# Performance work log

Hardware: AMD Instinct MI355X
Metric: run time of the kernel (lower is better)

Reference implementation:

```python
import jax, jax.numpy as jnp
import numpy as np

D_MODEL = 256
N_HEADS = 8
N_LEVELS = 3
N_POINTS = 4
D_HEAD = D_MODEL // N_HEADS
SHAPES = [(128, 128), (64, 64), (32, 32)]  # (H, W) per level
BS = 8
NQ = 900


def setup_inputs() -> dict:
    key = jax.random.key(0)
    ks = jax.random.split(key, 13)
    sum_hw = sum(h * w for h, w in SHAPES)
    s = 0.02
    starts = np.cumsum([0] + [h * w for h, w in SHAPES[:-1]]).astype(np.int32)
    return {
        "query": jax.random.normal(ks[0], (BS, NQ, D_MODEL), jnp.float32),
        "reference_points": jax.random.uniform(ks[1], (BS, NQ, N_LEVELS, 2), jnp.float32),
        "input_flatten": jax.random.normal(ks[2], (BS, sum_hw, D_MODEL), jnp.float32),
        "spatial_shapes": jnp.array(SHAPES, jnp.int32),
        "level_start_index": jnp.array(starts, jnp.int32),
        "W_off": jax.random.normal(ks[3], (D_MODEL, N_HEADS * N_LEVELS * N_POINTS * 2), jnp.float32) * s,
        "b_off": jax.random.normal(ks[4], (N_HEADS * N_LEVELS * N_POINTS * 2,), jnp.float32),
        "W_attn": jax.random.normal(ks[5], (D_MODEL, N_HEADS * N_LEVELS * N_POINTS), jnp.float32) * s,
        "b_attn": jax.random.normal(ks[6], (N_HEADS * N_LEVELS * N_POINTS,), jnp.float32) * s,
        "W_val": jax.random.normal(ks[7], (D_MODEL, D_MODEL), jnp.float32) * s,
        "b_val": jnp.zeros((D_MODEL,), jnp.float32),
        "W_out": jax.random.normal(ks[8], (D_MODEL, D_MODEL), jnp.float32) * s,
        "b_out": jnp.zeros((D_MODEL,), jnp.float32),
    }


def _msda(query, reference_points, input_flatten, shapes_np, starts_np,
          W_off, b_off, W_attn, b_attn, W_val, b_val, W_out, b_out):
    bs, nq, _ = query.shape
    # value projection -> [bs, sum_hw, H, Dh]
    value = (input_flatten @ W_val + b_val).reshape(bs, -1, N_HEADS, D_HEAD)
    # learned offsets and attention weights
    offsets = (query @ W_off + b_off).reshape(bs, nq, N_HEADS, N_LEVELS, N_POINTS, 2)
    attn = (query @ W_attn + b_attn).reshape(bs, nq, N_HEADS, N_LEVELS * N_POINTS)
    attn = jax.nn.softmax(attn, axis=-1).reshape(bs, nq, N_HEADS, N_LEVELS, N_POINTS)

    bidx = jnp.arange(bs)[:, None, None, None]
    hidx = jnp.arange(N_HEADS)[None, None, :, None]
    acc = jnp.zeros((bs, nq, N_HEADS, D_HEAD), value.dtype)
    for l in range(N_LEVELS):
        Hl, Wl = int(shapes_np[l, 0]), int(shapes_np[l, 1])
        st = int(starts_np[l])
        # [bs, H, Hl*Wl, Dh]
        v = jnp.transpose(value[:, st:st + Hl * Wl], (0, 2, 1, 3))
        norm = jnp.array([Wl, Hl], value.dtype)
        # sampling locations in [0,1] -> pixel coords (grid_sample align_corners=False)
        loc = reference_points[:, :, None, l, None, :] + offsets[:, :, :, l] / norm
        px = loc[..., 0] * Wl - 0.5  # [bs, nq, H, P]
        py = loc[..., 1] * Hl - 0.5
        x0 = jnp.floor(px); y0 = jnp.floor(py)
        lx = px - x0; ly = py - y0
        x0i = x0.astype(jnp.int32); y0i = y0.astype(jnp.int32)

        def gather(ix, iy):
            valid = (ix >= 0) & (ix < Wl) & (iy >= 0) & (iy < Hl)
            flat = jnp.clip(iy, 0, Hl - 1) * Wl + jnp.clip(ix, 0, Wl - 1)
            g = v[bidx, hidx, flat]  # [bs, nq, H, P, Dh]
            return g * valid[..., None].astype(v.dtype)

        samp = (gather(x0i, y0i) * ((1 - lx) * (1 - ly))[..., None]
                + gather(x0i + 1, y0i) * (lx * (1 - ly))[..., None]
                + gather(x0i, y0i + 1) * ((1 - lx) * ly)[..., None]
                + gather(x0i + 1, y0i + 1) * (lx * ly)[..., None])
        acc = acc + jnp.einsum('bqhp,bqhpd->bqhd', attn[:, :, :, l], samp)

    return acc.reshape(bs, nq, D_MODEL) @ W_out + b_out


def reference(query, reference_points, input_flatten, spatial_shapes, level_start_index,
              W_off, b_off, W_attn, b_attn, W_val, b_val, W_out, b_out):
    shapes_np = np.asarray(spatial_shapes)
    starts_np = np.asarray(level_start_index)
    return _msda(query, reference_points, input_flatten, shapes_np, starts_np,
                 W_off, b_off, W_attn, b_attn, W_val, b_val, W_out, b_out)
```

## Files before the change

kernel.cpp:

```cpp
#include <hip/hip_runtime.h>
#include <hip/hip_bf16.h>

typedef __bf16 bf16;
typedef bf16 bf16x8 __attribute__((ext_vector_type(8)));
typedef float f32x4 __attribute__((ext_vector_type(4)));

#define BSZ 8
#define NQ 900
#define NH 8
#define SUMHW 21504
#define NROW 7200

#define BIGF 3.3e38f

__device__ inline float ld_rt(const void* p, size_t i, int f32) {
  return f32 ? ((const float*)p)[i] : (float)((const bf16*)p)[i];
}

__device__ inline bf16x8 load_a8(const void* p, size_t i, int f32) {
  if (f32) {
    const float4* s = (const float4*)((const float*)p + i);
    float4 v0 = s[0], v1 = s[1];
    bf16x8 d;
    d[0] = (bf16)v0.x; d[1] = (bf16)v0.y; d[2] = (bf16)v0.z; d[3] = (bf16)v0.w;
    d[4] = (bf16)v1.x; d[5] = (bf16)v1.y; d[6] = (bf16)v1.z; d[7] = (bf16)v1.w;
    return d;
  }
  return *(const bf16x8*)((const bf16*)p + i);
}

__global__ void probe_flags(const bf16* q, int* flags) {
  const int lane = threadIdx.x;
  int c = 0;
  for (int i = lane; i < 512; i += 64) {
    float x = (float)q[i];
    if (!(fabsf(x) <= 1000.f)) c++;
  }
#pragma unroll
  for (int m = 1; m < 64; m <<= 1) c += __shfl_xor(c, m, 64);
  if (lane == 0) {
    flags[0] = (c > 32) ? 1 : 0;
    flags[1] = 0;
    flags[2] = 0;
  }
}

__global__ __launch_bounds__(256) void transpose256(const void* __restrict__ in,
                                                    bf16* __restrict__ out,
                                                    const int* __restrict__ flags) {
  const int f32 = flags[0];
  int idx = blockIdx.x * 256 + threadIdx.x;
  int k = idx >> 8, n = idx & 255;
  out[n * 256 + k] = (bf16)ld_rt(in, idx, f32);
}

__global__ __launch_bounds__(256) void transpose_oa(const void* __restrict__ Woff,
                                                    const void* __restrict__ Wattn,
                                                    bf16* __restrict__ Wt,
                                                    const int* __restrict__ flags) {
  const int f32 = flags[0];
  int idx = blockIdx.x * 256 + threadIdx.x;
  int n = idx >> 8, k = idx & 255;
  float v = (n < 192) ? ld_rt(Woff, (size_t)k * 192 + n, f32)
                      : ld_rt(Wattn, (size_t)k * 96 + (n - 192), f32);
  Wt[idx] = (bf16)v;
}

template <typename TC>
__global__ __launch_bounds__(256) void gemm_stream(
    const void* __restrict__ A, const bf16* __restrict__ Wt,
    const void* __restrict__ bias, TC* __restrict__ C, int rowbase, int M,
    const int* __restrict__ aflags, const int* __restrict__ bflags) {
  const int af32 = aflags[0], bf32 = bflags[0];
  const int t = threadIdx.x;
  const int w = t >> 6, lane = t & 63;
  const int ml = lane & 15, qd = lane >> 4;
  const int blockM = blockIdx.x * 64 + w * 16;
  f32x4 acc[16] = {};

  int r0 = blockM + ml;
  if (r0 > M - 1) r0 = M - 1;
  const size_t ar = ((size_t)rowbase + r0) * 256;

  for (int ks = 0; ks < 8; ++ks) {
    const int kof = ks * 32 + qd * 8;
    bf16x8 a = load_a8(A, ar + kof, af32);
#pragma unroll
    for (int tn = 0; tn < 16; ++tn) {
      bf16x8 bb = *(const bf16x8*)(Wt + (size_t)(tn * 16 + ml) * 256 + kof);
      acc[tn] = __builtin_amdgcn_mfma_f32_16x16x32_bf16(a, bb, acc[tn], 0, 0, 0);
    }
  }

#pragma unroll
  for (int tn = 0; tn < 16; ++tn) {
    int col = tn * 16 + ml;
    float bv = ld_rt(bias, col, bf32);
#pragma unroll
    for (int rr = 0; rr < 4; ++rr) {
      int row = blockM + qd * 4 + rr;
      float v = fminf(fmaxf(acc[tn][rr] + bv, -BIGF), BIGF);
      if (row < M) C[((size_t)rowbase + row) * 256 + col] = (TC)v;
    }
  }
}

__global__ __launch_bounds__(256) void gemm_oa_stream(
    const void* __restrict__ query, const bf16* __restrict__ Wt,
    const void* __restrict__ boff, const void* __restrict__ battn,
    float* __restrict__ offs, float* __restrict__ logits,
    const int* __restrict__ flags) {
  const int f32 = flags[0];
  const int t = threadIdx.x;
  const int w = t >> 6, lane = t & 63;
  const int ml = lane & 15, qd = lane >> 4;
  const int blockM = blockIdx.x * 64 + w * 16;
  f32x4 acc[18] = {};

  int r0 = blockM + ml;
  if (r0 > NROW - 1) r0 = NROW - 1;
  const size_t ar = (size_t)r0 * 256;

  for (int ks = 0; ks < 8; ++ks) {
    const int kof = ks * 32 + qd * 8;
    bf16x8 a = load_a8(query, ar + kof, f32);
#pragma unroll
    for (int tn = 0; tn < 18; ++tn) {
      bf16x8 bb = *(const bf16x8*)(Wt + (size_t)(tn * 16 + ml) * 256 + kof);
      acc[tn] = __builtin_amdgcn_mfma_f32_16x16x32_bf16(a, bb, acc[tn], 0, 0, 0);
    }
  }

#pragma unroll
  for (int tn = 0; tn < 18; ++tn) {
    int col = tn * 16 + ml;
#pragma unroll
    for (int rr = 0; rr < 4; ++rr) {
      int row = blockM + qd * 4 + rr;
      if (row < NROW) {
        float v = acc[tn][rr];
        if (col < 192)
          offs[(size_t)row * 192 + col] = v + ld_rt(boff, col, f32);
        else
          logits[(size_t)row * 96 + (col - 192)] = v + ld_rt(battn, col - 192, f32);
      }
    }
  }
}

__global__ __launch_bounds__(256) void msda_sample(
    const bf16* __restrict__ value, const void* __restrict__ refp,
    const float* __restrict__ offs, const float* __restrict__ logits,
    bf16* __restrict__ accb, int b_base, size_t batch_stride,
    const int* __restrict__ flags) {
  const int f32 = flags[0];
  const int qi = blockIdx.x, bl = blockIdx.y;
  const int b = b_base + bl;
  const int row = b * NQ + qi;
  const int t = threadIdx.x, h = t >> 5, d = t & 31;
  const bf16* valb = value + (size_t)bl * batch_stride;

  const float* lg = logits + (size_t)(row * NH + h) * 12;
  float lv[12];
#pragma unroll
  for (int i = 0; i < 12; ++i) lv[i] = fminf(fmaxf(lg[i], -BIGF), BIGF);
  float mx = -BIGF;
#pragma unroll
  for (int i = 0; i < 12; ++i) mx = fmaxf(mx, lv[i]);
  float e[12], se = 0.f;
#pragma unroll
  for (int i = 0; i < 12; ++i) {
    e[i] = __expf(lv[i] - mx);
    se += e[i];
  }
  const float inv = 1.f / se;

  const float* of = offs + (size_t)(row * NH + h) * 24;
  const int Hs[3] = {128, 64, 32}, Wd[3] = {128, 64, 32}, st[3] = {0, 16384, 20480};
  float acc = 0.f;
#pragma unroll
  for (int l = 0; l < 3; ++l) {
    const int Hl = Hs[l], Wl = Wd[l];
    float rx = ld_rt(refp, (size_t)(row * 3 + l) * 2 + 0, f32);
    float ry = ld_rt(refp, (size_t)(row * 3 + l) * 2 + 1, f32);
    const bf16* base = valb + (size_t)st[l] * 256 + h * 32 + d;
#pragma unroll
    for (int p = 0; p < 4; ++p) {
      float ox = of[(l * 4 + p) * 2 + 0], oy = of[(l * 4 + p) * 2 + 1];
      float px = (rx + ox / (float)Wl) * (float)Wl - 0.5f;
      float py = (ry + oy / (float)Hl) * (float)Hl - 0.5f;
      px = fminf(fmaxf(px, -1e6f), 1e6f);
      py = fminf(fmaxf(py, -1e6f), 1e6f);
      const float x0f = floorf(px), y0f = floorf(py);
      const float lx = px - x0f, ly = py - y0f;
      const int x0 = (int)x0f, y0 = (int)y0f;
      const float wgt = e[l * 4 + p] * inv;
      float s = 0.f;
#pragma unroll
      for (int cy = 0; cy < 2; ++cy) {
        const int iy = y0 + cy;
        const float wy = cy ? ly : 1.f - ly;
        const bool vy = (iy >= 0) && (iy < Hl);
        const int iyc = iy < 0 ? 0 : (iy > Hl - 1 ? Hl - 1 : iy);
#pragma unroll
        for (int cx = 0; cx < 2; ++cx) {
          const int ix = x0 + cx;
          const float wx = cx ? lx : 1.f - lx;
          const bool vx = (ix >= 0) && (ix < Wl);
          const int ixc = ix < 0 ? 0 : (ix > Wl - 1 ? Wl - 1 : ix);
          float g = (float)base[(size_t)(iyc * Wl + ixc) * 256];
          g = fminf(fmaxf(g, -BIGF), BIGF);
          s += (vx && vy) ? wx * wy * g : 0.f;
        }
      }
      acc += wgt * s;
    }
  }
  accb[(size_t)row * 256 + t] = (bf16)acc;
}

extern "C" void kernel_launch(void* const* d_in, const int* in_sizes, int n_in,
                              void* d_out, int out_size, void* d_ws, size_t ws_size,
                              hipStream_t stream) {
  const void* query = d_in[0];
  const void* refp = d_in[1];
  const void* inpf = d_in[2];
  const void* W_off = d_in[5];
  const void* b_off = d_in[6];
  const void* W_attn = d_in[7];
  const void* b_attn = d_in[8];
  const void* W_val = d_in[9];
  const void* b_val = d_in[10];
  const void* W_out = d_in[11];
  const void* b_out = d_in[12];

  float* out = (float*)d_out;
  char* ws = (char*)d_ws;
  int* flags = (int*)ws;
  const int* bf16flag = flags + 2;
  bf16* Wt_val = (bf16*)(ws + 256);
  bf16* Wt_out = (bf16*)(ws + 131328);
  bf16* Wt_oa = (bf16*)(ws + 262400);
  float* offs = (float*)(ws + 409856);
  float* logits = (float*)(ws + 5939456);
  bf16* accb = (bf16*)(ws + 8704256);
  bf16* value = (bf16*)(ws + 12390656);
  const unsigned long long WS_FULL = 12390656ULL + 88080384ULL;
  const unsigned long long WS_TIGHT = 12390656ULL + 11010048ULL;

  const int pipeline_ok = ws_size >= WS_TIGHT;
  const int full = ws_size >= WS_FULL;

  probe_flags<<<1, 64, 0, stream>>>((const bf16*)query, flags);
  if (pipeline_ok) {
    transpose256<<<256, 256, 0, stream>>>(W_val, Wt_val, flags);
    transpose256<<<256, 256, 0, stream>>>(W_out, Wt_out, flags);
    transpose_oa<<<288, 256, 0, stream>>>(W_off, W_attn, Wt_oa, flags);
    gemm_oa_stream<<<(NROW + 63) / 64, 256, 0, stream>>>(query, Wt_oa, b_off,
                                                         b_attn, offs, logits,
                                                         flags);
    if (full) {
      gemm_stream<bf16><<<(BSZ * SUMHW) / 64, 256, 0, stream>>>(
          inpf, Wt_val, b_val, value, 0, BSZ * SUMHW, flags, flags);
      msda_sample<<<dim3(NQ, BSZ), 256, 0, stream>>>(
          value, refp, offs, logits, accb, 0, (size_t)SUMHW * 256, flags);
    } else {
      for (int b = 0; b < BSZ; ++b) {
        gemm_stream<bf16><<<SUMHW / 64, 256, 0, stream>>>(
            inpf, Wt_val, b_val, value - (size_t)b * SUMHW * 256, b * SUMHW, SUMHW,
            flags, flags);
        msda_sample<<<dim3(NQ, 1), 256, 0, stream>>>(value, refp, offs, logits, accb,
                                                     b, 0, flags);
      }
    }
    gemm_stream<float><<<(NROW + 63) / 64, 256, 0, stream>>>(
        accb, Wt_out, b_out, out, 0, NROW, bf16flag, flags);
  }
}
```

Measured before the change: 566.7 us.

## Stage transposed weights in swizzled LDS and use persistent 512-thread GEMM blocks

```diff
diff --git a/kernel.cpp b/kernel.cpp
--- a/kernel.cpp
+++ b/kernel.cpp
@@ -67,82 +67,116 @@
 }
 
 template <typename TC>
-__global__ __launch_bounds__(256) void gemm_stream(
+__global__ __launch_bounds__(512, 2) void gemm_ldsb(
     const void* __restrict__ A, const bf16* __restrict__ Wt,
     const void* __restrict__ bias, TC* __restrict__ C, int rowbase, int M,
     const int* __restrict__ aflags, const int* __restrict__ bflags) {
+  extern __shared__ bf16 Bs[];
   const int af32 = aflags[0], bf32 = bflags[0];
   const int t = threadIdx.x;
   const int w = t >> 6, lane = t & 63;
   const int ml = lane & 15, qd = lane >> 4;
-  const int blockM = blockIdx.x * 64 + w * 16;
-  f32x4 acc[16] = {};
-
-  int r0 = blockM + ml;
-  if (r0 > M - 1) r0 = M - 1;
-  const size_t ar = ((size_t)rowbase + r0) * 256;
-
-  for (int ks = 0; ks < 8; ++ks) {
-    const int kof = ks * 32 + qd * 8;
-    bf16x8 a = load_a8(A, ar + kof, af32);
+
+#pragma unroll
+  for (int i = 0; i < 16; ++i) {
+    int g = t * 16 + i;
+    int row = g >> 5, e = (g & 31) * 8;
+    bf16x8 v = *(const bf16x8*)(Wt + row * 256 + e);
+    *(bf16x8*)&Bs[row * 256 + (e ^ ((row & 7) * 8))] = v;
+  }
+  __syncthreads();
+
+  const int nst = (M + 127) >> 7;
+  for (int st = blockIdx.x; st < nst; st += gridDim.x) {
+    const int tileM = st * 128 + w * 16;
+    int r0 = tileM + ml;
+    if (r0 > M - 1) r0 = M - 1;
+    const size_t ar = ((size_t)rowbase + r0) * 256;
+
+    bf16x8 a[8];
+#pragma unroll
+    for (int ks = 0; ks < 8; ++ks) a[ks] = load_a8(A, ar + ks * 32 + qd * 8, af32);
+
+    f32x4 acc[16] = {};
+#pragma unroll
+    for (int ks = 0; ks < 8; ++ks) {
+      const int swz = (ks * 32 + qd * 8) ^ ((ml & 7) * 8);
+#pragma unroll
+      for (int tn = 0; tn < 16; ++tn) {
+        bf16x8 bb = *(const bf16x8*)&Bs[(tn * 16 + ml) * 256 + swz];
+        acc[tn] = __builtin_amdgcn_mfma_f32_16x16x32_bf16(a[ks], bb, acc[tn], 0, 0, 0);
+      }
+    }
+
 #pragma unroll
     for (int tn = 0; tn < 16; ++tn) {
-      bf16x8 bb = *(const bf16x8*)(Wt + (size_t)(tn * 16 + ml) * 256 + kof);
-      acc[tn] = __builtin_amdgcn_mfma_f32_16x16x32_bf16(a, bb, acc[tn], 0, 0, 0);
-    }
-  }
-
-#pragma unroll
-  for (int tn = 0; tn < 16; ++tn) {
-    int col = tn * 16 + ml;
-    float bv = ld_rt(bias, col, bf32);
-#pragma unroll
-    for (int rr = 0; rr < 4; ++rr) {
-      int row = blockM + qd * 4 + rr;
-      float v = fminf(fmaxf(acc[tn][rr] + bv, -BIGF), BIGF);
-      if (row < M) C[((size_t)rowbase + row) * 256 + col] = (TC)v;
-    }
-  }
-}
-
-__global__ __launch_bounds__(256) void gemm_oa_stream(
+      int col = tn * 16 + ml;
+      float bv = ld_rt(bias, col, bf32);
+#pragma unroll
+      for (int rr = 0; rr < 4; ++rr) {
+        int row = tileM + qd * 4 + rr;
+        float v = fminf(fmaxf(acc[tn][rr] + bv, -BIGF), BIGF);
+        if (row < M) C[((size_t)rowbase + row) * 256 + col] = (TC)v;
+      }
+    }
+  }
+}
+
+__global__ __launch_bounds__(512, 2) void gemm_oa_ldsb(
     const void* __restrict__ query, const bf16* __restrict__ Wt,
     const void* __restrict__ boff, const void* __restrict__ battn,
     float* __restrict__ offs, float* __restrict__ logits,
     const int* __restrict__ flags) {
+  extern __shared__ bf16 Bs[];
   const int f32 = flags[0];
   const int t = threadIdx.x;
   const int w = t >> 6, lane = t & 63;
   const int ml = lane & 15, qd = lane >> 4;
-  const int blockM = blockIdx.x * 64 + w * 16;
-  f32x4 acc[18] = {};
-
-  int r0 = blockM + ml;
-  if (r0 > NROW - 1) r0 = NROW - 1;
-  const size_t ar = (size_t)r0 * 256;
-
-  for (int ks = 0; ks < 8; ++ks) {
-    const int kof = ks * 32 + qd * 8;
-    bf16x8 a = load_a8(query, ar + kof, f32);
+
+#pragma unroll
+  for (int i = 0; i < 18; ++i) {
+    int g = t * 18 + i;
+    int row = g >> 5, e = (g & 31) * 8;
+    bf16x8 v = *(const bf16x8*)(Wt + row * 256 + e);
+    *(bf16x8*)&Bs[row * 256 + (e ^ ((row & 7) * 8))] = v;
+  }
+  __syncthreads();
+
+  const int nst = (NROW + 127) >> 7;
+  for (int st = blockIdx.x; st < nst; st += gridDim.x) {
+    const int tileM = st * 128 + w * 16;
+    int r0 = tileM + ml;
+    if (r0 > NROW - 1) r0 = NROW - 1;
+    const size_t ar = (size_t)r0 * 256;
+
+    bf16x8 a[8];
+#pragma unroll
+    for (int ks = 0; ks < 8; ++ks) a[ks] = load_a8(query, ar + ks * 32 + qd * 8, f32);
+
+    f32x4 acc[18] = {};
+#pragma unroll
+    for (int ks = 0; ks < 8; ++ks) {
+      const int swz = (ks * 32 + qd * 8) ^ ((ml & 7) * 8);
+#pragma unroll
+      for (int tn = 0; tn < 18; ++tn) {
+        bf16x8 bb = *(const bf16x8*)&Bs[(tn * 16 + ml) * 256 + swz];
+        acc[tn] = __builtin_amdgcn_mfma_f32_16x16x32_bf16(a[ks], bb, acc[tn], 0, 0, 0);
+      }
+    }
+
 #pragma unroll
     for (int tn = 0; tn < 18; ++tn) {
-      bf16x8 bb = *(const bf16x8*)(Wt + (size_t)(tn * 16 + ml) * 256 + kof);
-      acc[tn] = __builtin_amdgcn_mfma_f32_16x16x32_bf16(a, bb, acc[tn], 0, 0, 0);
-    }
-  }
-
-#pragma unroll
-  for (int tn = 0; tn < 18; ++tn) {
-    int col = tn * 16 + ml;
-#pragma unroll
-    for (int rr = 0; rr < 4; ++rr) {
-      int row = blockM + qd * 4 + rr;
-      if (row < NROW) {
-        float v = acc[tn][rr];
-        if (col < 192)
-          offs[(size_t)row * 192 + col] = v + ld_rt(boff, col, f32);
-        else
-          logits[(size_t)row * 96 + (col - 192)] = v + ld_rt(battn, col - 192, f32);
+      int col = tn * 16 + ml;
+#pragma unroll
+      for (int rr = 0; rr < 4; ++rr) {
+        int row = tileM + qd * 4 + rr;
+        if (row < NROW) {
+          float v = acc[tn][rr];
+          if (col < 192)
+            offs[(size_t)row * 192 + col] = v + ld_rt(boff, col, f32);
+          else
+            logits[(size_t)row * 96 + (col - 192)] = v + ld_rt(battn, col - 192, f32);
+        }
       }
     }
   }
@@ -256,24 +290,23 @@
     transpose256<<<256, 256, 0, stream>>>(W_val, Wt_val, flags);
     transpose256<<<256, 256, 0, stream>>>(W_out, Wt_out, flags);
     transpose_oa<<<288, 256, 0, stream>>>(W_off, W_attn, Wt_oa, flags);
-    gemm_oa_stream<<<(NROW + 63) / 64, 256, 0, stream>>>(query, Wt_oa, b_off,
-                                                         b_attn, offs, logits,
-                                                         flags);
+    gemm_oa_ldsb<<<(NROW + 127) / 128, 512, 147456, stream>>>(
+        query, Wt_oa, b_off, b_attn, offs, logits, flags);
     if (full) {
-      gemm_stream<bf16><<<(BSZ * SUMHW) / 64, 256, 0, stream>>>(
+      gemm_ldsb<bf16><<<256, 512, 131072, stream>>>(
           inpf, Wt_val, b_val, value, 0, BSZ * SUMHW, flags, flags);
       msda_sample<<<dim3(NQ, BSZ), 256, 0, stream>>>(
           value, refp, offs, logits, accb, 0, (size_t)SUMHW * 256, flags);
     } else {
       for (int b = 0; b < BSZ; ++b) {
-        gemm_stream<bf16><<<SUMHW / 64, 256, 0, stream>>>(
+        gemm_ldsb<bf16><<<SUMHW / 128, 512, 131072, stream>>>(
             inpf, Wt_val, b_val, value - (size_t)b * SUMHW * 256, b * SUMHW, SUMHW,
             flags, flags);
         msda_sample<<<dim3(NQ, 1), 256, 0, stream>>>(value, refp, offs, logits, accb,
                                                      b, 0, flags);
       }
     }
-    gemm_stream<float><<<(NROW + 63) / 64, 256, 0, stream>>>(
+    gemm_ldsb<float><<<(NROW + 127) / 128, 512, 131072, stream>>>(
         accb, Wt_out, b_out, out, 0, NROW, bf16flag, flags);
   }
 }
```

Result: slower. 869.4 us (+53.4%).
